# Kernel tuning notes

Measured on AMD Instinct MI355X. Metric: run time of the kernel, lower is better.

The kernel has to match this reference:

```python
import jax, jax.numpy as jnp
import numpy as np

HEADS, DH, M_LAND, PINV_ITERS, LN_EPS = 8, 64, 256, 6, 1e-5


def layer_norm(x, g, b):
    mu = x.mean(-1, keepdims=True)
    var = ((x - mu) ** 2).mean(-1, keepdims=True)
    return (x - mu) * jax.lax.rsqrt(var + LN_EPS) * g + b


def moore_penrose_pinv(x, iters=PINV_ITERS):
    # x: (h, m, m). Iterative Newton-Schulz style pinv (lucidrains).
    abs_x = jnp.abs(x)
    col = abs_x.sum(-1)
    row = abs_x.sum(-2)
    z = jnp.swapaxes(x, -1, -2) / (jnp.max(col) * jnp.max(row))
    I = jnp.eye(x.shape[-1], dtype=x.dtype)
    for _ in range(iters):
        xz = x @ z
        z = 0.25 * z @ (13.0 * I - xz @ (15.0 * I - xz @ (7.0 * I - xz)))
    return z


def nystrom_attention(x, qkv_w, out_w, out_b, res_w):
    # x: (n, dim). No mask, eval mode (dropout off).
    n, dim = x.shape
    pad = (-n) % M_LAND
    xp = jnp.pad(x, ((pad, 0), (0, 0)))  # pad at sequence START, as in original
    n_p = n + pad
    l = n_p // M_LAND  # tokens per landmark
    qkv = xp @ qkv_w  # (n_p, 3*h*dh)
    q, k, v = jnp.split(qkv, 3, axis=-1)
    split = lambda t: t.reshape(n_p, HEADS, DH).transpose(1, 0, 2)  # (h, n_p, dh)
    q, k, v = split(q), split(k), split(v)
    q = q * (DH ** -0.5)
    q_l = q.reshape(HEADS, M_LAND, l, DH).mean(axis=2)  # (h, m, dh)
    k_l = k.reshape(HEADS, M_LAND, l, DH).mean(axis=2)
    sim1 = jnp.einsum('hid,hjd->hij', q, k_l)    # (h, n_p, m)
    sim2 = jnp.einsum('hid,hjd->hij', q_l, k_l)  # (h, m, m)
    sim3 = jnp.einsum('hid,hjd->hij', q_l, k)    # (h, m, n_p)
    a1 = jax.nn.softmax(sim1, axis=-1)
    a2 = jax.nn.softmax(sim2, axis=-1)
    a3 = jax.nn.softmax(sim3, axis=-1)
    a2_inv = moore_penrose_pinv(a2)
    out = a1 @ (a2_inv @ (a3 @ v))  # (h, n_p, dh)
    # residual depthwise conv over sequence dim, kernel 33, per head
    res = jax.lax.conv_general_dilated(
        v[None], res_w, (1, 1), ((16, 16), (0, 0)),
        feature_group_count=HEADS, dimension_numbers=('NCHW', 'OIHW', 'NCHW'))[0]
    out = out + res
    out = out.transpose(1, 0, 2).reshape(n_p, HEADS * DH)
    out = out @ out_w + out_b
    return out[-n:]  # drop the leading pad


def ppeg(x, w7, b7, w5, b5, w3, b3, H, W):
    cls_tok, feat = x[0], x[1:]
    C = feat.shape[1]
    img = feat.T.reshape(1, C, H, W)
    def dw(w, b, p):
        y = jax.lax.conv_general_dilated(
            img, w, (1, 1), ((p, p), (p, p)),
            feature_group_count=C, dimension_numbers=('NCHW', 'OIHW', 'NCHW'))
        return y + b.reshape(1, C, 1, 1)
    out = img + dw(w7, b7, 3) + dw(w5, b5, 2) + dw(w3, b3, 1)
    out = out[0].reshape(C, H * W).T
    return jnp.concatenate([cls_tok[None], out], axis=0)


def forward(h, fc1_w, fc1_b, cls_token, l1_ln_g, l1_ln_b, l1_qkv_w, l1_out_w, l1_out_b, l1_res_w,
            conv7_w, conv7_b, conv5_w, conv5_b, conv3_w, conv3_b,
            l2_ln_g, l2_ln_b, l2_qkv_w, l2_out_w, l2_out_b, l2_res_w,
            norm_g, norm_b, fc2_w, fc2_b):
    x = jax.nn.relu(h @ fc1_w + fc1_b)  # (N, 512)
    N = x.shape[0]
    Hs = Ws = int(np.ceil(np.sqrt(N)))  # N chosen perfect square -> add_length == 0
    x = jnp.concatenate([cls_token, x], axis=0)  # (N+1, 512)
    x = x + nystrom_attention(layer_norm(x, l1_ln_g, l1_ln_b), l1_qkv_w, l1_out_w, l1_out_b, l1_res_w)
    x = ppeg(x, conv7_w, conv7_b, conv5_w, conv5_b, conv3_w, conv3_b, Hs, Ws)
    x = x + nystrom_attention(layer_norm(x, l2_ln_g, l2_ln_b), l2_qkv_w, l2_out_w, l2_out_b, l2_res_w)
    x = layer_norm(x, norm_g, norm_b)[0]  # cls token readout
    return x @ fc2_w + fc2_b  # (n_classes,)


def setup_inputs() -> dict:
    key = jax.random.key(0)
    ks = jax.random.split(key, 16)
    nrm = lambda k, s, sc=0.02: jax.random.normal(k, s, jnp.float32) * sc
    D = 512
    return {
        'h': jax.random.normal(ks[0], (16384, 2048), jnp.float32),
        'fc1_w': nrm(ks[1], (2048, D)), 'fc1_b': jnp.zeros((D,), jnp.float32),
        'cls_token': nrm(ks[2], (1, D), 1.0),
        'l1_ln_g': jnp.ones((D,), jnp.float32), 'l1_ln_b': jnp.zeros((D,), jnp.float32),
        'l1_qkv_w': nrm(ks[3], (D, 3 * D)),
        'l1_out_w': nrm(ks[4], (D, D)), 'l1_out_b': jnp.zeros((D,), jnp.float32),
        'l1_res_w': nrm(ks[5], (HEADS, 1, 33, 1), 0.05),
        'conv7_w': nrm(ks[6], (D, 1, 7, 7), 0.05), 'conv7_b': jnp.zeros((D,), jnp.float32),
        'conv5_w': nrm(ks[7], (D, 1, 5, 5), 0.05), 'conv5_b': jnp.zeros((D,), jnp.float32),
        'conv3_w': nrm(ks[8], (D, 1, 3, 3), 0.05), 'conv3_b': jnp.zeros((D,), jnp.float32),
        'l2_ln_g': jnp.ones((D,), jnp.float32), 'l2_ln_b': jnp.zeros((D,), jnp.float32),
        'l2_qkv_w': nrm(ks[9], (D, 3 * D)),
        'l2_out_w': nrm(ks[10], (D, D)), 'l2_out_b': jnp.zeros((D,), jnp.float32),
        'l2_res_w': nrm(ks[11], (HEADS, 1, 33, 1), 0.05),
        'norm_g': jnp.ones((D,), jnp.float32), 'norm_b': jnp.zeros((D,), jnp.float32),
        'fc2_w': nrm(ks[12], (D, 2)), 'fc2_b': jnp.zeros((2,), jnp.float32),
    }


def reference(h, fc1_w, fc1_b, cls_token, l1_ln_g, l1_ln_b, l1_qkv_w, l1_out_w, l1_out_b, l1_res_w,
              conv7_w, conv7_b, conv5_w, conv5_b, conv3_w, conv3_b,
              l2_ln_g, l2_ln_b, l2_qkv_w, l2_out_w, l2_out_b, l2_res_w,
              norm_g, norm_b, fc2_w, fc2_b):
    return forward(h, fc1_w, fc1_b, cls_token, l1_ln_g, l1_ln_b, l1_qkv_w, l1_out_w, l1_out_b, l1_res_w,
                   conv7_w, conv7_b, conv5_w, conv5_b, conv3_w, conv3_b,
                   l2_ln_g, l2_ln_b, l2_qkv_w, l2_out_w, l2_out_b, l2_res_w,
                   norm_g, norm_b, fc2_w, fc2_b)
```

## Files before the change

### kernel.cpp

```cpp
#include <hip/hip_runtime.h>
#include <cstddef>

#define NROWS 16385
#define NPAD  16640
#define PADT  255
#define DIM   512
#define HEADS 8
#define DH    64
#define NL    256
#define LCH   65
#define LCHUNK 65
#define SLACK 24
#define LDST  40
#define AST   72

typedef short bf16x8 __attribute__((ext_vector_type(8)));
typedef float f32x4  __attribute__((ext_vector_type(4)));

__device__ __forceinline__ float wsum(float v){
#pragma unroll
  for (int o = 32; o; o >>= 1) v += __shfl_xor(v, o);
  return v;
}
__device__ __forceinline__ float wmax(float v){
#pragma unroll
  for (int o = 32; o; o >>= 1) v = fmaxf(v, __shfl_xor(v, o));
  return v;
}

__device__ __forceinline__ int xcd_swz(int orig, int nwg){
  int q = nwg >> 3, r = nwg & 7;
  int x = orig & 7, j = orig >> 3;
  return (x < r ? x*(q+1) : r*(q+1) + (x-r)*q) + j;
}

__device__ __forceinline__ void split2(float x, unsigned short &h, unsigned short &l){
  unsigned ux = __float_as_uint(x);
  unsigned rh = (ux + 0x7FFFu + ((ux >> 16) & 1u)) >> 16;
  h = (unsigned short)rh;
  float fh = __uint_as_float(rh << 16);
  float r = x - fh;
  unsigned ur = __float_as_uint(r);
  unsigned rl = (ur + 0x7FFFu + ((ur >> 16) & 1u)) >> 16;
  l = (unsigned short)rl;
}
__device__ __forceinline__ float bf2f(unsigned short h){
  return __uint_as_float((unsigned)h << 16);
}

__global__ __launch_bounds__(256) void gemm64_sp_kernel(
    const unsigned short* __restrict__ Ah, const unsigned short* __restrict__ Al,
    const unsigned short* __restrict__ Bth, const unsigned short* __restrict__ Btl,
    const unsigned short* __restrict__ IB1h, const unsigned short* __restrict__ IB1l,
    const unsigned short* __restrict__ IB2h, const unsigned short* __restrict__ IB2l,
    float* __restrict__ Cf,
    unsigned short* __restrict__ Crh, unsigned short* __restrict__ Crl,
    unsigned short* __restrict__ Cth, unsigned short* __restrict__ Ctl,
    int M, int N, int K, long sA, long sB, long sC,
    float aAcc, float cDiag, float c1, float c2)
{
  size_t zo = (size_t)blockIdx.z;
  Ah  += zo*sA; Al  += zo*sA;
  Bth += zo*sB; Btl += zo*sB;
  if (IB1h){ IB1h += zo*sA; IB1l += zo*sA; }
  if (IB2h){ IB2h += zo*sA; IB2l += zo*sA; }
  if (Cf)  Cf  += zo*sC;
  if (Crh){ Crh += zo*sC; Crl += zo*sC; }
  if (Cth){ Cth += zo*sC; Ctl += zo*sC; }
  __shared__ unsigned short LAh[64*LDST], LAl[64*LDST], LBh[64*LDST], LBl[64*LDST];
  const int t = threadIdx.x;
  const int wid = t >> 6, lane = t & 63;
  const int wr = wid >> 1, wc = wid & 1;
  const int l15 = lane & 15, kb = lane >> 4;
  const int bm = blockIdx.y << 6, bn = blockIdx.x << 6;
  const int r4 = t >> 2, kc = (t & 3) << 3;
  f32x4 acc[2][2];
#pragma unroll
  for (int i=0;i<2;++i)
#pragma unroll
    for (int j=0;j<2;++j) acc[i][j] = (f32x4){0.f,0.f,0.f,0.f};

  for (int k0 = 0; k0 < K; k0 += 32){
    __syncthreads();
    {
      int lo = r4*LDST + kc;
      *(uint4*)&LAh[lo] = *(const uint4*)&Ah[(size_t)(bm+r4)*K + k0 + kc];
      *(uint4*)&LAl[lo] = *(const uint4*)&Al[(size_t)(bm+r4)*K + k0 + kc];
      *(uint4*)&LBh[lo] = *(const uint4*)&Bth[(size_t)(bn+r4)*K + k0 + kc];
      *(uint4*)&LBl[lo] = *(const uint4*)&Btl[(size_t)(bn+r4)*K + k0 + kc];
    }
    __syncthreads();
    bf16x8 ah[2], al[2], bh[2], bl[2];
#pragma unroll
    for (int r=0;r<2;++r){
      int off = (wr*32 + r*16 + l15)*LDST + kb*8;
      ah[r] = *(const bf16x8*)&LAh[off];
      al[r] = *(const bf16x8*)&LAl[off];
    }
#pragma unroll
    for (int c2v=0;c2v<2;++c2v){
      int off = (wc*32 + c2v*16 + l15)*LDST + kb*8;
      bh[c2v] = *(const bf16x8*)&LBh[off];
      bl[c2v] = *(const bf16x8*)&LBl[off];
    }
#pragma unroll
    for (int r=0;r<2;++r)
#pragma unroll
      for (int c2v=0;c2v<2;++c2v){
        acc[r][c2v] = __builtin_amdgcn_mfma_f32_16x16x32_bf16(ah[r], bh[c2v], acc[r][c2v], 0,0,0);
        acc[r][c2v] = __builtin_amdgcn_mfma_f32_16x16x32_bf16(ah[r], bl[c2v], acc[r][c2v], 0,0,0);
        acc[r][c2v] = __builtin_amdgcn_mfma_f32_16x16x32_bf16(al[r], bh[c2v], acc[r][c2v], 0,0,0);
      }
  }
#pragma unroll
  for (int r=0;r<2;++r){
#pragma unroll
    for (int c2v=0;c2v<2;++c2v){
      int col = bn + wc*32 + c2v*16 + l15;
      int rb  = bm + wr*32 + r*16 + kb*4;
      float v[4];
#pragma unroll
      for (int e=0;e<4;++e){
        float x = aAcc*acc[r][c2v][e];
        int row = rb + e;
        if (cDiag != 0.f && row == col) x += cDiag;
        if (IB1h){
          size_t io = (size_t)row*K + col;
          x += c1*(bf2f(IB1h[io]) + bf2f(IB1l[io]));
        }
        if (IB2h){
          size_t io = (size_t)row*K + col;
          x += c2*(bf2f(IB2h[io]) + bf2f(IB2l[io]));
        }
        v[e] = x;
      }
      if (Cf){
#pragma unroll
        for (int e=0;e<4;++e) Cf[(size_t)(rb+e)*N + col] = v[e];
      }
      if (Crh){
#pragma unroll
        for (int e=0;e<4;++e){
          unsigned short hh, ll;
          split2(v[e], hh, ll);
          Crh[(size_t)(rb+e)*N + col] = hh;
          Crl[(size_t)(rb+e)*N + col] = ll;
        }
      }
      if (Cth){
        unsigned short h4[4], l4[4];
#pragma unroll
        for (int e=0;e<4;++e) split2(v[e], h4[e], l4[e]);
        uint2 uh, ul;
        uh.x = (unsigned)h4[0] | ((unsigned)h4[1]<<16);
        uh.y = (unsigned)h4[2] | ((unsigned)h4[3]<<16);
        ul.x = (unsigned)l4[0] | ((unsigned)l4[1]<<16);
        ul.y = (unsigned)l4[2] | ((unsigned)l4[3]<<16);
        *(uint2*)&Cth[(size_t)col*M + rb] = uh;
        *(uint2*)&Ctl[(size_t)col*M + rb] = ul;
      }
    }
  }
}

__global__ __launch_bounds__(256) void gemm_sb_kernel(
    const unsigned short* __restrict__ Ah, const unsigned short* __restrict__ Al,
    const unsigned short* __restrict__ BTh, const unsigned short* __restrict__ BTl,
    const float* __restrict__ bias, float* __restrict__ C,
    int M, int N, int K, int accum)
{
  __shared__ unsigned short LAh[128*LDST], LAl[128*LDST], LBh[128*LDST], LBl[128*LDST];
  const int t = threadIdx.x;
  const int nwg = gridDim.x * gridDim.y;
  const int orig = blockIdx.y * gridDim.x + blockIdx.x;
  const int wgid = xcd_swz(orig, nwg);
  const int bxi = wgid % gridDim.x, byi = wgid / gridDim.x;
  const int bm = byi << 7, bn = bxi << 7;
  const int wid = t >> 6, lane = t & 63;
  const int wr = wid >> 1, wc = wid & 1;
  const int l15 = lane & 15, kb = lane >> 4;
  const int sr = t >> 1, sc0 = (t & 1) << 4;
  f32x4 acc[4][4];
#pragma unroll
  for (int i=0;i<4;++i)
#pragma unroll
    for (int j=0;j<4;++j) acc[i][j] = (f32x4){0.f,0.f,0.f,0.f};

  const uint4 zz = make_uint4(0,0,0,0);
  for (int k0 = 0; k0 < K; k0 += 32){
    __syncthreads();
    {
      bool av = (bm + sr) < M;
      size_t ga = (size_t)(bm + sr)*K + k0 + sc0;
      uint4 a0 = av ? *(const uint4*)(Ah + ga)     : zz;
      uint4 a1 = av ? *(const uint4*)(Ah + ga + 8) : zz;
      uint4 a2 = av ? *(const uint4*)(Al + ga)     : zz;
      uint4 a3 = av ? *(const uint4*)(Al + ga + 8) : zz;
      size_t gb = (size_t)(bn + sr)*K + k0 + sc0;
      uint4 b0 = *(const uint4*)(BTh + gb);
      uint4 b1 = *(const uint4*)(BTh + gb + 8);
      uint4 b2 = *(const uint4*)(BTl + gb);
      uint4 b3 = *(const uint4*)(BTl + gb + 8);
      int lo = sr*LDST + sc0;
      *(uint4*)&LAh[lo] = a0; *(uint4*)&LAh[lo+8] = a1;
      *(uint4*)&LAl[lo] = a2; *(uint4*)&LAl[lo+8] = a3;
      *(uint4*)&LBh[lo] = b0; *(uint4*)&LBh[lo+8] = b1;
      *(uint4*)&LBl[lo] = b2; *(uint4*)&LBl[lo+8] = b3;
    }
    __syncthreads();
    bf16x8 ah[4], al[4], bh[4], bl[4];
#pragma unroll
    for (int ai=0; ai<4; ++ai){
      int off = (wr*64 + ai*16 + l15)*LDST + kb*8;
      ah[ai] = *(const bf16x8*)&LAh[off];
      al[ai] = *(const bf16x8*)&LAl[off];
    }
#pragma unroll
    for (int bj=0; bj<4; ++bj){
      int off = (wc*64 + bj*16 + l15)*LDST + kb*8;
      bh[bj] = *(const bf16x8*)&LBh[off];
      bl[bj] = *(const bf16x8*)&LBl[off];
    }
#pragma unroll
    for (int ai=0; ai<4; ++ai)
#pragma unroll
      for (int bj=0; bj<4; ++bj){
        acc[ai][bj] = __builtin_amdgcn_mfma_f32_16x16x32_bf16(ah[ai], bh[bj], acc[ai][bj], 0,0,0);
        acc[ai][bj] = __builtin_amdgcn_mfma_f32_16x16x32_bf16(ah[ai], bl[bj], acc[ai][bj], 0,0,0);
        acc[ai][bj] = __builtin_amdgcn_mfma_f32_16x16x32_bf16(al[ai], bh[bj], acc[ai][bj], 0,0,0);
      }
  }
#pragma unroll
  for (int ai=0; ai<4; ++ai){
#pragma unroll
    for (int bj=0; bj<4; ++bj){
      int col = bn + wc*64 + bj*16 + l15;
      float bv = bias ? bias[col] : 0.f;
#pragma unroll
      for (int r=0; r<4; ++r){
        int row = bm + wr*64 + ai*16 + kb*4 + r;
        if (row < M){
          float v = acc[ai][bj][r] + bv;
          if (accum) v += C[(size_t)row*N + col];
          C[(size_t)row*N + col] = v;
        }
      }
    }
  }
}

__global__ __launch_bounds__(256) void gemm_sbf_kernel(
    const float* __restrict__ A,
    const unsigned short* __restrict__ BTh, const unsigned short* __restrict__ BTl,
    const float* __restrict__ bias, float* __restrict__ C,
    int M, int N, int K, int relu)
{
  __shared__ unsigned short LAh[128*LDST], LAl[128*LDST], LBh[128*LDST], LBl[128*LDST];
  const int t = threadIdx.x;
  const int nwg = gridDim.x * gridDim.y;
  const int orig = blockIdx.y * gridDim.x + blockIdx.x;
  const int wgid = xcd_swz(orig, nwg);
  const int bxi = wgid % gridDim.x, byi = wgid / gridDim.x;
  const int bm = byi << 7, bn = bxi << 7;
  const int wid = t >> 6, lane = t & 63;
  const int wr = wid >> 1, wc = wid & 1;
  const int l15 = lane & 15, kb = lane >> 4;
  const int sr = t >> 1, sc0 = (t & 1) << 4;
  f32x4 acc[4][4];
#pragma unroll
  for (int i=0;i<4;++i)
#pragma unroll
    for (int j=0;j<4;++j) acc[i][j] = (f32x4){0.f,0.f,0.f,0.f};

  for (int k0 = 0; k0 < K; k0 += 32){
    __syncthreads();
    {
      const float* ap = A + (size_t)(bm + sr)*K + k0 + sc0;
      float va[16];
      *(float4*)&va[0]  = ((const float4*)ap)[0];
      *(float4*)&va[4]  = ((const float4*)ap)[1];
      *(float4*)&va[8]  = ((const float4*)ap)[2];
      *(float4*)&va[12] = ((const float4*)ap)[3];
      int lo = sr*LDST + sc0;
      unsigned* dh = (unsigned*)&LAh[lo];
      unsigned* dl = (unsigned*)&LAl[lo];
#pragma unroll
      for (int q=0;q<8;++q){
        unsigned short h0,l0,h1,l1;
        split2(va[2*q],   h0, l0);
        split2(va[2*q+1], h1, l1);
        dh[q] = (unsigned)h0 | ((unsigned)h1 << 16);
        dl[q] = (unsigned)l0 | ((unsigned)l1 << 16);
      }
      size_t gb = (size_t)(bn + sr)*K + k0 + sc0;
      uint4 b0 = *(const uint4*)(BTh + gb);
      uint4 b1 = *(const uint4*)(BTh + gb + 8);
      uint4 b2 = *(const uint4*)(BTl + gb);
      uint4 b3 = *(const uint4*)(BTl + gb + 8);
      *(uint4*)&LBh[lo] = b0; *(uint4*)&LBh[lo+8] = b1;
      *(uint4*)&LBl[lo] = b2; *(uint4*)&LBl[lo+8] = b3;
    }
    __syncthreads();
    bf16x8 ah[4], al[4], bh[4], bl[4];
#pragma unroll
    for (int ai=0; ai<4; ++ai){
      int off = (wr*64 + ai*16 + l15)*LDST + kb*8;
      ah[ai] = *(const bf16x8*)&LAh[off];
      al[ai] = *(const bf16x8*)&LAl[off];
    }
#pragma unroll
    for (int bj=0; bj<4; ++bj){
      int off = (wc*64 + bj*16 + l15)*LDST + kb*8;
      bh[bj] = *(const bf16x8*)&LBh[off];
      bl[bj] = *(const bf16x8*)&LBl[off];
// ... 19 lines not shown
        float v = acc[ai][bj][r] + bv;
        if (relu) v = fmaxf(v, 0.f);
        C[(size_t)row*N + col] = v;
      }
    }
  }
}

__global__ void wt_split_T_kernel(const float* __restrict__ W,
                                  unsigned short* __restrict__ BTh,
                                  unsigned short* __restrict__ BTl, int K, int N)
{
  int idx = blockIdx.x*256 + threadIdx.x;
  if (idx >= N*K) return;
  int n = idx / K, k = idx - n*K;
  unsigned short h, l;
  split2(W[(size_t)k*N + n], h, l);
  BTh[idx] = h; BTl[idx] = l;
}

__global__ void att_split_kernel(const float* __restrict__ ATT,
                                 unsigned short* __restrict__ Ah,
                                 unsigned short* __restrict__ Al)
{
  size_t i4 = (size_t)blockIdx.x*256 + threadIdx.x;
  size_t e = i4*4;
  int row = (int)(e >> 9);
  float4 v = make_float4(0.f,0.f,0.f,0.f);
  if (row < NROWS) v = *(const float4*)(ATT + (size_t)PADT*DIM + e);
  unsigned short h0,l0,h1,l1,h2,l2,h3,l3;
  split2(v.x,h0,l0); split2(v.y,h1,l1); split2(v.z,h2,l2); split2(v.w,h3,l3);
  uint2 uh, ul;
  uh.x = (unsigned)h0 | ((unsigned)h1<<16); uh.y = (unsigned)h2 | ((unsigned)h3<<16);
  ul.x = (unsigned)l0 | ((unsigned)l1<<16); ul.y = (unsigned)l2 | ((unsigned)l3<<16);
  *(uint2*)(Ah + e) = uh;
  *(uint2*)(Al + e) = ul;
}

__global__ __launch_bounds__(256) void ln_pad_sb_kernel(
    const float* __restrict__ X, const float* __restrict__ g,
    const float* __restrict__ b, unsigned short* __restrict__ Yh,
    unsigned short* __restrict__ Yl)
{
  int p = blockIdx.x;
  int t = threadIdx.x;
  size_t base = (size_t)p*DIM;
  if (p < PADT){
    Yh[base+t] = 0; Yh[base+t+256] = 0;
    Yl[base+t] = 0; Yl[base+t+256] = 0;
    return;
  }
  const float* xr = X + (size_t)(p-PADT)*DIM;
  float x0 = xr[t], x1 = xr[t+256];
  float s = x0 + x1, sq = x0*x0 + x1*x1;
  s = wsum(s); sq = wsum(sq);
  __shared__ float rs[4], rq[4];
  if ((t&63)==0){ rs[t>>6]=s; rq[t>>6]=sq; }
  __syncthreads();
  float S = rs[0]+rs[1]+rs[2]+rs[3];
  float SQ = rq[0]+rq[1]+rq[2]+rq[3];
  float mu = S * (1.f/DIM);
  float var = SQ * (1.f/DIM) - mu*mu;
  float r = rsqrtf(var + 1e-5f);
  float y0 = (x0-mu)*r*g[t]     + b[t];
  float y1 = (x1-mu)*r*g[t+256] + b[t+256];
  unsigned short h, l;
  split2(y0, h, l); Yh[base+t] = h;     Yl[base+t] = l;
  split2(y1, h, l); Yh[base+t+256] = h; Yl[base+t+256] = l;
}

__global__ void landmarks_kernel(const float* __restrict__ QKV,
                                 float* __restrict__ QL, float* __restrict__ KL,
                                 unsigned short* __restrict__ KLh,
                                 unsigned short* __restrict__ KLl)
{
  int m = blockIdx.x, h = blockIdx.y, d = threadIdx.x;
  float sq = 0.f, sk = 0.f;
  const float* base = QKV + (size_t)(m*LCH)*1536 + (h<<6) + d;
  for (int j = 0; j < LCH; ++j){
    sq += base[0];
    sk += base[512];
    base += 1536;
  }
  size_t off = (((size_t)(h<<8)+m)<<6) + d;
  float klv = sk * (1.f/65.f);
  QL[off] = sq * (0.125f/65.f);
  KL[off] = klv;
  unsigned short hh, ll;
  split2(klv, hh, ll);
  KLh[off] = hh; KLl[off] = ll;
}

__global__ __launch_bounds__(256) void sim2_kernel(
    const float* __restrict__ QL, const float* __restrict__ KL, float* __restrict__ A2)
{
  int m = blockIdx.x, h = blockIdx.y, n = threadIdx.x;
  __shared__ float ql[64];
  __shared__ float red[4];
  if (n < 64) ql[n] = QL[(((h<<8)+m)<<6) + n];
  __syncthreads();
  const float* kl = KL + (size_t)(((h<<8)+n)<<6);
  float s = 0.f;
#pragma unroll
  for (int d=0; d<64; ++d) s += ql[d]*kl[d];
  float mx = wmax(s);
  if ((n&63)==0) red[n>>6] = mx;
  __syncthreads();
  mx = fmaxf(fmaxf(red[0],red[1]), fmaxf(red[2],red[3]));
  float e = __expf(s - mx);
  float sm = wsum(e);
  __syncthreads();
  if ((n&63)==0) red[n>>6] = sm;
  __syncthreads();
  sm = red[0]+red[1]+red[2]+red[3];
  A2[((size_t)((h<<8)+m)<<8) + n] = e/sm;
}

__global__ void crsum_kernel(const float* __restrict__ A2, float* __restrict__ CR)
{
  int b = blockIdx.x, t = threadIdx.x;
  float v;
  if (b < 2048){
    v = fabsf(A2[((size_t)b<<8) + t]);
  } else {
    int r = b - 2048;
    int h = r >> 8, n = r & 255;
    v = fabsf(A2[((size_t)h<<16) + (t<<8) + n]);
  }
  v = wsum(v);
  __shared__ float red[4];
  if ((t&63)==0) red[t>>6]=v;
  __syncthreads();
  if (t==0) CR[b] = red[0]+red[1]+red[2]+red[3];
}
__global__ void maxprod_kernel(const float* __restrict__ CR, float* __restrict__ SCAL)
{
  int t = threadIdx.x;
  float mc = -3e38f, mr = -3e38f;
  for (int i=t; i<2048; i+=256){ mc = fmaxf(mc, CR[i]); mr = fmaxf(mr, CR[2048+i]); }
  mc = wmax(mc); mr = wmax(mr);
  __shared__ float rc[4], rr[4];
  if ((t&63)==0){ rc[t>>6]=mc; rr[t>>6]=mr; }
  __syncthreads();
  if (t==0){
    float a = fmaxf(fmaxf(rc[0],rc[1]),fmaxf(rc[2],rc[3]));
    float b = fmaxf(fmaxf(rr[0],rr[1]),fmaxf(rr[2],rr[3]));
    SCAL[0] = 1.f/(a*b);
  }
}

__global__ void tsplit_kernel(const float* __restrict__ A2, const float* __restrict__ SCAL,
                              unsigned short* __restrict__ A2h, unsigned short* __restrict__ A2l,
                              unsigned short* __restrict__ Zrh, unsigned short* __restrict__ Zrl,
                              unsigned short* __restrict__ Zth, unsigned short* __restrict__ Ztl)
{
  int idx = blockIdx.x*256 + threadIdx.x;
  int h = idx >> 16, rem = idx & 65535, m = rem >> 8, n = rem & 255;
  float a = A2[idx];
  unsigned short hh, ll;
  split2(a, hh, ll);
  A2h[idx] = hh; A2l[idx] = ll;
  float z = a * SCAL[0];
  split2(z, hh, ll);
  Zth[idx] = hh; Ztl[idx] = ll;
  size_t rmo = ((size_t)h<<16) + (n<<8) + m;
  Zrh[rmo] = hh; Zrl[rmo] = ll;
}

__global__ __launch_bounds__(256) void lattn3_kernel(
    const float* __restrict__ QKV, const float* __restrict__ QL,
    float* __restrict__ PACC, float* __restrict__ PML)
{
  const int c = blockIdx.x, lg = blockIdx.y, h = blockIdx.z;
  const int t = threadIdx.x;
  const int w = t >> 6, lane = t & 63;
  const int l15 = lane & 15, kb = lane >> 4;
  __shared__ unsigned short LQh[64*AST], LQl[64*AST];
  __shared__ unsigned short LKh[64*AST], LKl[64*AST];
  __shared__ unsigned short LPh[64*AST], LPl[64*AST];
  const int sr = t >> 2, sc0 = (t & 3) << 4;
  {
    const float* qp = QL + (((size_t)(h*256 + lg*64 + sr)) << 6) + sc0;
    float va[16];
    *(float4*)&va[0]  = ((const float4*)qp)[0];
    *(float4*)&va[4]  = ((const float4*)qp)[1];
    *(float4*)&va[8]  = ((const float4*)qp)[2];
    *(float4*)&va[12] = ((const float4*)qp)[3];
    unsigned* dh = (unsigned*)&LQh[sr*AST + sc0];
    unsigned* dl = (unsigned*)&LQl[sr*AST + sc0];
#pragma unroll
    for (int q=0;q<8;++q){
      unsigned short h0,l0,h1,l1;
      split2(va[2*q],   h0, l0);
      split2(va[2*q+1], h1, l1);
      dh[q] = (unsigned)h0 | ((unsigned)h1 << 16);
      dl[q] = (unsigned)l0 | ((unsigned)l1 << 16);
    }
  }
  float m = -3e38f, l = 0.f;
  f32x4 oacc[4];
#pragma unroll
  for (int i=0;i<4;++i) oacc[i] = (f32x4){0.f,0.f,0.f,0.f};

  for (int s = 0; s < 4; ++s){
    const int kbase = c*256 + s*64;
    __syncthreads();
    {
      const float* kp = QKV + (size_t)(kbase + sr)*1536 + 512 + (h<<6) + sc0;
      float va[16];
      *(float4*)&va[0]  = ((const float4*)kp)[0];
      *(float4*)&va[4]  = ((const float4*)kp)[1];
      *(float4*)&va[8]  = ((const float4*)kp)[2];
      *(float4*)&va[12] = ((const float4*)kp)[3];
      unsigned* dh = (unsigned*)&LKh[sr*AST + sc0];
      unsigned* dl = (unsigned*)&LKl[sr*AST + sc0];
#pragma unroll
      for (int q=0;q<8;++q){
        unsigned short h0,l0,h1,l1;
        split2(va[2*q],   h0, l0);
        split2(va[2*q+1], h1, l1);
        dh[q] = (unsigned)h0 | ((unsigned)h1 << 16);
        dl[q] = (unsigned)l0 | ((unsigned)l1 << 16);
      }
    }
    __syncthreads();
    f32x4 sacc[4];
#pragma unroll
    for (int i=0;i<4;++i) sacc[i] = (f32x4){0.f,0.f,0.f,0.f};
    __builtin_amdgcn_s_setprio(1);
#pragma unroll
    for (int ks = 0; ks < 2; ++ks){
      int qoff = (w*16 + l15)*AST + ks*32 + kb*8;
      bf16x8 bh = *(const bf16x8*)&LQh[qoff];
      bf16x8 bl = *(const bf16x8*)&LQl[qoff];
#pragma unroll
      for (int mi=0; mi<4; ++mi){
        int aoff = (mi*16 + l15)*AST + ks*32 + kb*8;
        bf16x8 ah = *(const bf16x8*)&LKh[aoff];
        bf16x8 al = *(const bf16x8*)&LKl[aoff];
        sacc[mi] = __builtin_amdgcn_mfma_f32_16x16x32_bf16(ah, bh, sacc[mi], 0,0,0);
        sacc[mi] = __builtin_amdgcn_mfma_f32_16x16x32_bf16(ah, bl, sacc[mi], 0,0,0);
        sacc[mi] = __builtin_amdgcn_mfma_f32_16x16x32_bf16(al, bh, sacc[mi], 0,0,0);
      }
    }
    __builtin_amdgcn_s_setprio(0);
    float tm = -3e38f;
#pragma unroll
    for (int mi=0;mi<4;++mi)
#pragma unroll
      for (int e=0;e<4;++e) tm = fmaxf(tm, sacc[mi][e]);
    tm = fmaxf(tm, __shfl_xor(tm, 16));
    tm = fmaxf(tm, __shfl_xor(tm, 32));
    float Mn = fmaxf(m, tm);
    float sc = __expf(m - Mn);
    float ts = 0.f;
    float p[4][4];
#pragma unroll
    for (int mi=0;mi<4;++mi)
#pragma unroll
      for (int e=0;e<4;++e){
        float pv = __expf(sacc[mi][e] - Mn);
        p[mi][e] = pv; ts += pv;
      }
    ts += __shfl_xor(ts, 16);
    ts += __shfl_xor(ts, 32);
    l = l*sc + ts;
    m = Mn;
#pragma unroll
    for (int mi=0;mi<4;++mi)
#pragma unroll
      for (int e=0;e<4;++e) oacc[mi][e] *= sc;
#pragma unroll
    for (int mi=0;mi<4;++mi){
      unsigned short h4[4], l4[4];
#pragma unroll
      for (int e=0;e<4;++e) split2(p[mi][e], h4[e], l4[e]);
      uint2 uh, ul;
      uh.x = (unsigned)h4[0] | ((unsigned)h4[1]<<16);
      uh.y = (unsigned)h4[2] | ((unsigned)h4[3]<<16);
      ul.x = (unsigned)l4[0] | ((unsigned)l4[1]<<16);
      ul.y = (unsigned)l4[2] | ((unsigned)l4[3]<<16);
      int po = (w*16 + l15)*AST + mi*16 + kb*4;
      *(uint2*)&LPh[po] = uh;
      *(uint2*)&LPl[po] = ul;
    }
    __syncthreads();
    {
      const float* vp = QKV + (size_t)(kbase + sr)*1536 + 1024 + (h<<6) + sc0;
      float va[16];
      *(float4*)&va[0]  = ((const float4*)vp)[0];
      *(float4*)&va[4]  = ((const float4*)vp)[1];
      *(float4*)&va[8]  = ((const float4*)vp)[2];
      *(float4*)&va[12] = ((const float4*)vp)[3];
#pragma unroll
      for (int i=0;i<16;++i){
        unsigned short hh, ll;
        split2(va[i], hh, ll);
        LKh[(sc0+i)*AST + sr] = hh;
        LKl[(sc0+i)*AST + sr] = ll;
      }
    }
    __syncthreads();
    __builtin_amdgcn_s_setprio(1);
#pragma unroll
    for (int ks = 0; ks < 2; ++ks){
      int poff = (w*16 + l15)*AST + ks*32 + kb*8;
      bf16x8 pbh = *(const bf16x8*)&LPh[poff];
      bf16x8 pbl = *(const bf16x8*)&LPl[poff];
#pragma unroll
// ... 207 lines not shown
    }
  }
}

__global__ void zero_slack_kernel(float* __restrict__ QKV)
{
  int i = blockIdx.x*256 + threadIdx.x;
  QKV[(size_t)NPAD*1536 + i] = 0.f;
}

__global__ __launch_bounds__(256) void convres2_kernel(
    const float* __restrict__ QKV, const float* __restrict__ rw,
    float* __restrict__ ATT)
{
  const int t = threadIdx.x;
  const int c = blockIdx.y*256 + t;
  const int i0 = PADT + (blockIdx.x << 2);
  const int h = c >> 6;
  float w[33];
#pragma unroll
  for (int k=0;k<33;++k) w[k] = rw[h*33 + k];
  float acc[4] = {0.f,0.f,0.f,0.f};
  const float* vbase = QKV + (size_t)(i0-16)*1536 + 1024 + c;
#pragma unroll
  for (int rr=0; rr<36; ++rr){
    float v = vbase[(size_t)rr*1536];
#pragma unroll
    for (int k=0;k<4;++k){
      int tap = rr - k;
      if (tap >= 0 && tap <= 32) acc[k] += w[tap]*v;
    }
  }
#pragma unroll
  for (int k=0;k<4;++k){
    int i = i0 + k;
    if (i < NPAD) ATT[(size_t)i*DIM + c] += acc[k];
  }
}

__global__ void pad_kernel(const float* __restrict__ X, float* __restrict__ PIM)
{
  int r = blockIdx.x;
  int c = blockIdx.y*256 + threadIdx.x;
  int py = r / 134, px = r - py*134;
  float v = 0.f;
  if (py>=3 && py<131 && px>=3 && px<131)
    v = X[(size_t)(1 + (py-3)*128 + (px-3))*512 + c];
  PIM[(size_t)r*512 + c] = v;
}

__global__ void wtrans_kernel(const float* __restrict__ w7, const float* __restrict__ w5,
                              const float* __restrict__ w3, float* __restrict__ W7T,
                              float* __restrict__ W5T, float* __restrict__ W3T)
{
  int i = blockIdx.x;
  int c = blockIdx.y*256 + threadIdx.x;
  if (i < 49)      W7T[i*512+c]      = w7[c*49+i];
  else if (i < 74) W5T[(i-49)*512+c] = w5[c*25+(i-49)];
  else             W3T[(i-74)*512+c] = w3[c*9+(i-74)];
}

__global__ __launch_bounds__(256) void ppeg2_kernel(
    const float* __restrict__ PIM, const float* __restrict__ W7T,
    const float* __restrict__ W5T, const float* __restrict__ W3T,
    const float* __restrict__ b7, const float* __restrict__ b5,
    const float* __restrict__ b3, float* __restrict__ X2)
{
  const int t = threadIdx.x;
  const int c = blockIdx.z*256 + t;
  const int x = blockIdx.x;
  const int y0 = blockIdx.y << 2;
  float w7r[49], w5r[25], w3r[9];
#pragma unroll
  for (int i=0;i<49;++i) w7r[i] = W7T[i*512 + c];
#pragma unroll
  for (int i=0;i<25;++i) w5r[i] = W5T[i*512 + c];
#pragma unroll
  for (int i=0;i<9;++i)  w3r[i] = W3T[i*512 + c];
  const float bsum = b7[c] + b5[c] + b3[c];
  float acc[4] = {bsum, bsum, bsum, bsum};
  const float* base = PIM + ((size_t)(y0*134 + x))*512 + c;
#pragma unroll
  for (int rr=0; rr<10; ++rr){
#pragma unroll
    for (int cc=0; cc<7; ++cc){
      float v = base[(size_t)(rr*134 + cc)*512];
#pragma unroll
      for (int k=0;k<4;++k){
        const int dy = rr - k - 3, dx = cc - 3;
        if (dy >= -3 && dy <= 3){
          acc[k] += w7r[(dy+3)*7 + (dx+3)] * v;
          if (dy >= -2 && dy <= 2 && dx >= -2 && dx <= 2)
            acc[k] += w5r[(dy+2)*5 + (dx+2)] * v;
          if (dy >= -1 && dy <= 1 && dx >= -1 && dx <= 1)
            acc[k] += w3r[(dy+1)*3 + (dx+1)] * v;
          if (dy == 0 && dx == 0) acc[k] += v;
        }
      }
    }
  }
#pragma unroll
  for (int k=0;k<4;++k)
    X2[(size_t)(1 + (y0+k)*128 + x)*512 + c] = acc[k];
}

__global__ void copy_row_kernel(const float* __restrict__ src, float* __restrict__ dst)
{
  dst[threadIdx.x] = src[threadIdx.x];
}

__global__ void final_kernel(const float* __restrict__ X, const float* __restrict__ g,
                             const float* __restrict__ b, const float* __restrict__ fw,
                             const float* __restrict__ fb, float* __restrict__ out)
{
  int t = threadIdx.x;
  float x0 = X[t], x1 = X[t+256];
  float s = x0 + x1, sq = x0*x0 + x1*x1;
  s = wsum(s); sq = wsum(sq);
  __shared__ float rs[4], rq[4];
  if ((t&63)==0){ rs[t>>6]=s; rq[t>>6]=sq; }
  __syncthreads();
  float S = rs[0]+rs[1]+rs[2]+rs[3];
  float SQ = rq[0]+rq[1]+rq[2]+rq[3];
  float mu = S*(1.f/DIM);
  float var = SQ*(1.f/DIM) - mu*mu;
  float r = rsqrtf(var + 1e-5f);
  float n0 = (x0-mu)*r*g[t]     + b[t];
  float n1 = (x1-mu)*r*g[t+256] + b[t+256];
  float p0 = n0*fw[t*2]   + n1*fw[(t+256)*2];
  float p1 = n0*fw[t*2+1] + n1*fw[(t+256)*2+1];
  p0 = wsum(p0); p1 = wsum(p1);
  __shared__ float r0[4], r1[4];
  if ((t&63)==0){ r0[t>>6]=p0; r1[t>>6]=p1; }
  __syncthreads();
  if (t==0){
    out[0] = r0[0]+r0[1]+r0[2]+r0[3] + fb[0];
    out[1] = r1[0]+r1[1]+r1[2]+r1[3] + fb[1];
  }
}

struct Bufs {
  float *Y, *QKV, *QL, *KL, *A2, *CR, *SCAL, *PACC, *PML, *W7T, *W5T, *W3T;
  unsigned short *Yh, *Yl, *ATh, *ATl, *qBTh, *qBTl, *oBTh, *oBTl, *fBTh, *fBTl;
  unsigned short *A2h, *A2l, *XZrh, *XZrl, *XZth, *XZtl, *Wth, *Wtl, *W2th, *W2tl;
  unsigned short *Z0rh, *Z0rl, *Z0th, *Z0tl, *Z1rh, *Z1rl, *Z1th, *Z1tl;
  unsigned short *TMth, *TMtl, *KLh, *KLl, *BMth, *BMtl;
};

static void attention_layer(float* X, const float* ln_g, const float* ln_b,
                            const float* qkv_w, const float* out_w, const float* out_b,
                            const float* res_w, Bufs& bf, hipStream_t stream)
{
  const long SP = 65536;
  wt_split_T_kernel<<<(1536*512)/256, 256, 0, stream>>>(qkv_w, bf.qBTh, bf.qBTl, 512, 1536);
  wt_split_T_kernel<<<(512*512)/256, 256, 0, stream>>>(out_w, bf.oBTh, bf.oBTl, 512, 512);
  ln_pad_sb_kernel<<<NPAD, 256, 0, stream>>>(X, ln_g, ln_b, bf.Yh, bf.Yl);
  gemm_sb_kernel<<<dim3(12,130),256,0,stream>>>(bf.Yh, bf.Yl, bf.qBTh, bf.qBTl,
      nullptr, bf.QKV, NPAD, 1536, 512, 0);
  landmarks_kernel<<<dim3(NL,HEADS),64,0,stream>>>(bf.QKV, bf.QL, bf.KL, bf.KLh, bf.KLl);
  sim2_kernel<<<dim3(NL,HEADS),256,0,stream>>>(bf.QL, bf.KL, bf.A2);
  crsum_kernel<<<4096,256,0,stream>>>(bf.A2, bf.CR);
  maxprod_kernel<<<1,256,0,stream>>>(bf.CR, bf.SCAL);
  tsplit_kernel<<<2048,256,0,stream>>>(bf.A2, bf.SCAL, bf.A2h, bf.A2l,
      bf.Z0rh, bf.Z0rl, bf.Z0th, bf.Z0tl);
  unsigned short *Zarh=bf.Z0rh, *Zarl=bf.Z0rl, *Zath=bf.Z0th, *Zatl=bf.Z0tl;
  unsigned short *Zbrh=bf.Z1rh, *Zbrl=bf.Z1rl, *Zbth=bf.Z1th, *Zbtl=bf.Z1tl;
  for (int it = 0; it < 6; ++it){
    gemm64_sp_kernel<<<dim3(4,4,8),256,0,stream>>>(bf.A2h, bf.A2l, Zath, Zatl,
        nullptr,nullptr, nullptr,nullptr, nullptr,
        bf.XZrh, bf.XZrl, bf.XZth, bf.XZtl,
        256,256,256, SP,SP,SP, 1.f, 0.f, 0.f, 0.f);
    gemm64_sp_kernel<<<dim3(4,4,8),256,0,stream>>>(bf.XZrh, bf.XZrl, bf.XZth, bf.XZtl,
        bf.XZrh, bf.XZrl, nullptr,nullptr, nullptr,
        nullptr, nullptr, bf.Wth, bf.Wtl,
        256,256,256, SP,SP,SP, -1.f, 0.f, 7.f, 0.f);
    gemm64_sp_kernel<<<dim3(4,4,8),256,0,stream>>>(bf.XZrh, bf.XZrl, bf.Wth, bf.Wtl,
        bf.XZrh, bf.XZrl, nullptr,nullptr, nullptr,
        nullptr, nullptr, bf.W2th, bf.W2tl,
        256,256,256, SP,SP,SP, -1.f, 0.f, 15.f, 0.f);
    gemm64_sp_kernel<<<dim3(4,4,8),256,0,stream>>>(Zarh, Zarl, bf.W2th, bf.W2tl,
        Zarh, Zarl, nullptr,nullptr, nullptr,
        Zbrh, Zbrl, Zbth, Zbtl,
        256,256,256, SP,SP,SP, -0.25f, 0.f, 3.25f, 0.f);
    unsigned short* tp;
    tp=Zarh; Zarh=Zbrh; Zbrh=tp;  tp=Zarl; Zarl=Zbrl; Zbrl=tp;
    tp=Zath; Zath=Zbth; Zbth=tp;  tp=Zatl; Zatl=Zbtl; Zbtl=tp;
  }
  lattn3_kernel<<<dim3(LCHUNK,4,HEADS),256,0,stream>>>(bf.QKV, bf.QL, bf.PACC, bf.PML);
  lattn_combine_kernel<<<2048,64,0,stream>>>(bf.PACC, bf.PML, bf.TMth, bf.TMtl);
  gemm64_sp_kernel<<<dim3(1,4,8),256,0,stream>>>(Zarh, Zarl, bf.TMth, bf.TMtl,
      nullptr,nullptr, nullptr,nullptr, nullptr,
      nullptr, nullptr, bf.BMth, bf.BMtl,
      256,64,256, SP, 16384L, 16384L, 1.f, 0.f, 0.f, 0.f);
  float* ATT = bf.Y;
  attn3_kernel<<<dim3(257,HEADS),256,0,stream>>>(bf.QKV, bf.KLh, bf.KLl,
      bf.BMth, bf.BMtl, ATT);
  convres2_kernel<<<dim3(4097,2),256,0,stream>>>(bf.QKV, res_w, ATT);
  att_split_kernel<<<8256,256,0,stream>>>(ATT, bf.ATh, bf.ATl);
  gemm_sb_kernel<<<dim3(4,129),256,0,stream>>>(bf.ATh, bf.ATl, bf.oBTh, bf.oBTl,
      out_b, X, NROWS, 512, 512, 1);
}

extern "C" void kernel_launch(void* const* d_in, const int* in_sizes, int n_in,
                              void* d_out, int out_size, void* d_ws, size_t ws_size,
                              hipStream_t stream)
{
  (void)in_sizes; (void)n_in; (void)out_size; (void)ws_size;
  const float* h       = (const float*)d_in[0];
  const float* fc1_w   = (const float*)d_in[1];
  const float* fc1_b   = (const float*)d_in[2];
  const float* cls     = (const float*)d_in[3];
  const float* l1_ln_g = (const float*)d_in[4];
  const float* l1_ln_b = (const float*)d_in[5];
  const float* l1_qkv_w= (const float*)d_in[6];
  const float* l1_out_w= (const float*)d_in[7];
  const float* l1_out_b= (const float*)d_in[8];
  const float* l1_res_w= (const float*)d_in[9];
  const float* conv7_w = (const float*)d_in[10];
  const float* conv7_b = (const float*)d_in[11];
  const float* conv5_w = (const float*)d_in[12];
  const float* conv5_b = (const float*)d_in[13];
  const float* conv3_w = (const float*)d_in[14];
  const float* conv3_b = (const float*)d_in[15];
  const float* l2_ln_g = (const float*)d_in[16];
  const float* l2_ln_b = (const float*)d_in[17];
  const float* l2_qkv_w= (const float*)d_in[18];
  const float* l2_out_w= (const float*)d_in[19];
  const float* l2_out_b= (const float*)d_in[20];
  const float* l2_res_w= (const float*)d_in[21];
  const float* norm_g  = (const float*)d_in[22];
  const float* norm_b  = (const float*)d_in[23];
  const float* fc2_w   = (const float*)d_in[24];
  const float* fc2_b   = (const float*)d_in[25];

  float* ws = (float*)d_ws;
  float* X   = ws;                 ws += (size_t)NROWS*DIM;
  float* X2  = ws;                 ws += (size_t)NROWS*DIM;
  Bufs bf;
  bf.Y    = ws;                    ws += (size_t)NPAD*DIM;
  bf.QKV  = ws;                    ws += (size_t)(NPAD+SLACK)*1536;
  bf.QL   = ws;                    ws += HEADS*NL*DH;
  bf.KL   = ws;                    ws += HEADS*NL*DH;
  bf.A2   = ws;                    ws += HEADS*NL*NL;
  bf.CR   = ws;                    ws += 4096;
  bf.SCAL = ws;                    ws += 8;
  bf.PACC = ws;                    ws += (size_t)LCHUNK*HEADS*NL*DH;
  bf.PML  = ws;                    ws += (size_t)LCHUNK*HEADS*NL*2;
  bf.W7T  = ws;                    ws += 49*512;
  bf.W5T  = ws;                    ws += 25*512;
  bf.W3T  = ws;                    ws += 9*512;
  unsigned short* us = (unsigned short*)ws;
  bf.Yh   = us;                    us += (size_t)NPAD*DIM;
  bf.Yl   = us;                    us += (size_t)NPAD*DIM;
  bf.ATh  = us;                    us += (size_t)16512*DIM;
  bf.ATl  = us;                    us += (size_t)16512*DIM;
  bf.qBTh = us;                    us += 1536*512;
  bf.qBTl = us;                    us += 1536*512;
  bf.oBTh = us;                    us += 512*512;
  bf.oBTl = us;                    us += 512*512;
  bf.fBTh = us;                    us += 512*2048;
  bf.fBTl = us;                    us += 512*2048;
  const size_t PL = (size_t)HEADS*NL*NL;
  bf.A2h  = us; us += PL;  bf.A2l  = us; us += PL;
  bf.XZrh = us; us += PL;  bf.XZrl = us; us += PL;
  bf.XZth = us; us += PL;  bf.XZtl = us; us += PL;
  bf.Wth  = us; us += PL;  bf.Wtl  = us; us += PL;
  bf.W2th = us; us += PL;  bf.W2tl = us; us += PL;
  bf.Z0rh = us; us += PL;  bf.Z0rl = us; us += PL;
  bf.Z0th = us; us += PL;  bf.Z0tl = us; us += PL;
  bf.Z1rh = us; us += PL;  bf.Z1rl = us; us += PL;
  bf.Z1th = us; us += PL;  bf.Z1tl = us; us += PL;
  bf.TMth = us; us += (size_t)HEADS*NL*DH;
  bf.TMtl = us; us += (size_t)HEADS*NL*DH;
  bf.KLh  = us; us += (size_t)HEADS*NL*DH;
  bf.KLl  = us; us += (size_t)HEADS*NL*DH;
  bf.BMth = us; us += (size_t)HEADS*NL*DH;
  bf.BMtl = us; us += (size_t)HEADS*NL*DH;
  float* PIM = bf.QKV;

  zero_slack_kernel<<<(SLACK*1536)/256, 256, 0, stream>>>(bf.QKV);
  wtrans_kernel<<<dim3(83,2),256,0,stream>>>(conv7_w, conv5_w, conv3_w,
                                             bf.W7T, bf.W5T, bf.W3T);

  wt_split_T_kernel<<<(512*2048)/256, 256, 0, stream>>>(fc1_w, bf.fBTh, bf.fBTl, 2048, 512);
  gemm_sbf_kernel<<<dim3(4,128),256,0,stream>>>(h, bf.fBTh, bf.fBTl, fc1_b, X + DIM,
      16384, 512, 2048, 1);
  copy_row_kernel<<<1,512,0,stream>>>(cls, X);

  attention_layer(X, l1_ln_g, l1_ln_b, l1_qkv_w, l1_out_w, l1_out_b, l1_res_w, bf, stream);

  pad_kernel<<<dim3(17956,2),256,0,stream>>>(X, PIM);
  ppeg2_kernel<<<dim3(128,32,2),256,0,stream>>>(PIM, bf.W7T, bf.W5T, bf.W3T,
                                                conv7_b, conv5_b, conv3_b, X2);
  copy_row_kernel<<<1,512,0,stream>>>(X, X2);

  attention_layer(X2, l2_ln_g, l2_ln_b, l2_qkv_w, l2_out_w, l2_out_b, l2_res_w, bf, stream);

  final_kernel<<<1,256,0,stream>>>(X2, norm_g, norm_b, fc2_w, fc2_b, (float*)d_out);
}
```

Before: 1.913 ms.

## Fuse pinv Newton-Schulz iterations into one persistent kernel with grid barriers

Replaces the 24 small per-iteration GEMM launches of the Moore-Penrose pinv with a single persistent kernel of 128 blocks that runs all four stages of each of the six iterations. The stages are separated by an atomic-counter grid barrier, and the counter is reset in tsplit. The goal is to remove launch overhead and inter-kernel gaps on tiny 256x256 batched GEMMs. The cost is spin-wait barriers that assume all 128 blocks are co-resident, plus a risk of deadlock or memory-visibility problems. The final Z lands back in the Z0 buffers after an even number of swaps.

Result: slower. 2.958 ms (+54.6%).

```diff
diff --git a/kernel.cpp b/kernel.cpp
--- a/kernel.cpp
+++ b/kernel.cpp
@@ -46,6 +46,17 @@
 }
 __device__ __forceinline__ float bf2f(unsigned short h){
   return __uint_as_float((unsigned)h << 16);
+}
+
+__device__ __forceinline__ void gbar(unsigned* bar, unsigned target){
+  __threadfence();
+  __syncthreads();
+  if (threadIdx.x == 0){
+    atomicAdd(bar, 1u);
+    while (atomicAdd(bar, 0u) < target) __builtin_amdgcn_s_sleep(2);
+  }
+  __syncthreads();
+  __threadfence();
 }
 
 __global__ __launch_bounds__(256) void gemm64_sp_kernel(
@@ -160,6 +171,141 @@
         *(uint2*)&Ctl[(size_t)col*M + rb] = ul;
       }
     }
+  }
+}
+
+__device__ void pinv_stage(
+    const unsigned short* Ah, const unsigned short* Al,
+    const unsigned short* Bth, const unsigned short* Btl,
+    const unsigned short* IBh, const unsigned short* IBl,
+    unsigned short* Crh, unsigned short* Crl,
+    unsigned short* Cth, unsigned short* Ctl,
+    float aAcc, float c1, int bx, int by, int bz)
+{
+  __shared__ unsigned short LAh[64*LDST], LAl[64*LDST], LBh[64*LDST], LBl[64*LDST];
+  const size_t zo = (size_t)bz * 65536;
+  Ah += zo; Al += zo; Bth += zo; Btl += zo;
+  if (IBh){ IBh += zo; IBl += zo; }
+  if (Crh){ Crh += zo; Crl += zo; }
+  if (Cth){ Cth += zo; Ctl += zo; }
+  const int t = threadIdx.x;
+  const int wid = t >> 6, lane = t & 63;
+  const int wr = wid >> 1, wc = wid & 1;
+  const int l15 = lane & 15, kb = lane >> 4;
+  const int bm = by << 6, bn = bx << 6;
+  const int r4 = t >> 2, kc = (t & 3) << 3;
+  f32x4 acc[2][2];
+#pragma unroll
+  for (int i=0;i<2;++i)
+#pragma unroll
+    for (int j=0;j<2;++j) acc[i][j] = (f32x4){0.f,0.f,0.f,0.f};
+
+  for (int k0 = 0; k0 < 256; k0 += 32){
+    __syncthreads();
+    {
+      int lo = r4*LDST + kc;
+      *(uint4*)&LAh[lo] = *(const uint4*)&Ah[(size_t)(bm+r4)*256 + k0 + kc];
+      *(uint4*)&LAl[lo] = *(const uint4*)&Al[(size_t)(bm+r4)*256 + k0 + kc];
+      *(uint4*)&LBh[lo] = *(const uint4*)&Bth[(size_t)(bn+r4)*256 + k0 + kc];
+      *(uint4*)&LBl[lo] = *(const uint4*)&Btl[(size_t)(bn+r4)*256 + k0 + kc];
+    }
+    __syncthreads();
+    bf16x8 ah[2], al[2], bh[2], bl[2];
+#pragma unroll
+    for (int r=0;r<2;++r){
+      int off = (wr*32 + r*16 + l15)*LDST + kb*8;
+      ah[r] = *(const bf16x8*)&LAh[off];
+      al[r] = *(const bf16x8*)&LAl[off];
+    }
+#pragma unroll
+    for (int c2v=0;c2v<2;++c2v){
+      int off = (wc*32 + c2v*16 + l15)*LDST + kb*8;
+      bh[c2v] = *(const bf16x8*)&LBh[off];
+      bl[c2v] = *(const bf16x8*)&LBl[off];
+    }
+#pragma unroll
+    for (int r=0;r<2;++r)
+#pragma unroll
+      for (int c2v=0;c2v<2;++c2v){
+        acc[r][c2v] = __builtin_amdgcn_mfma_f32_16x16x32_bf16(ah[r], bh[c2v], acc[r][c2v], 0,0,0);
+        acc[r][c2v] = __builtin_amdgcn_mfma_f32_16x16x32_bf16(ah[r], bl[c2v], acc[r][c2v], 0,0,0);
+        acc[r][c2v] = __builtin_amdgcn_mfma_f32_16x16x32_bf16(al[r], bh[c2v], acc[r][c2v], 0,0,0);
+      }
+  }
+#pragma unroll
+  for (int r=0;r<2;++r){
+#pragma unroll
+    for (int c2v=0;c2v<2;++c2v){
+      int col = bn + wc*32 + c2v*16 + l15;
+      int rb  = bm + wr*32 + r*16 + kb*4;
+      float v[4];
+#pragma unroll
+      for (int e=0;e<4;++e){
+        float x = aAcc*acc[r][c2v][e];
+        if (IBh){
+          size_t io = (size_t)(rb+e)*256 + col;
+          x += c1*(bf2f(IBh[io]) + bf2f(IBl[io]));
+        }
+        v[e] = x;
+      }
+      if (Crh){
+#pragma unroll
+        for (int e=0;e<4;++e){
+          unsigned short hh, ll;
+          split2(v[e], hh, ll);
+          Crh[(size_t)(rb+e)*256 + col] = hh;
+          Crl[(size_t)(rb+e)*256 + col] = ll;
+        }
+      }
+      if (Cth){
+        unsigned short h4[4], l4[4];
+#pragma unroll
+        for (int e=0;e<4;++e) split2(v[e], h4[e], l4[e]);
+        uint2 uh, ul;
+        uh.x = (unsigned)h4[0] | ((unsigned)h4[1]<<16);
+        uh.y = (unsigned)h4[2] | ((unsigned)h4[3]<<16);
+        ul.x = (unsigned)l4[0] | ((unsigned)l4[1]<<16);
+        ul.y = (unsigned)l4[2] | ((unsigned)l4[3]<<16);
+        *(uint2*)&Cth[(size_t)col*256 + rb] = uh;
+        *(uint2*)&Ctl[(size_t)col*256 + rb] = ul;
+      }
+    }
+  }
+}
+
+__global__ __launch_bounds__(256) void pinv_fused_kernel(
+    const unsigned short* __restrict__ A2h, const unsigned short* __restrict__ A2l,
+    unsigned short* __restrict__ XZrh, unsigned short* __restrict__ XZrl,
+    unsigned short* __restrict__ XZth, unsigned short* __restrict__ XZtl,
+    unsigned short* __restrict__ Wth,  unsigned short* __restrict__ Wtl,
+    unsigned short* __restrict__ W2th, unsigned short* __restrict__ W2tl,
+    unsigned short* __restrict__ Z0rh, unsigned short* __restrict__ Z0rl,
+    unsigned short* __restrict__ Z0th, unsigned short* __restrict__ Z0tl,
+    unsigned short* __restrict__ Z1rh, unsigned short* __restrict__ Z1rl,
+    unsigned short* __restrict__ Z1th, unsigned short* __restrict__ Z1tl,
+    unsigned* __restrict__ bar)
+{
+  const int blk = blockIdx.x;
+  const int bx = blk & 3, by = (blk >> 2) & 3, bz = blk >> 4;
+  unsigned short *Zarh=Z0rh, *Zarl=Z0rl, *Zath=Z0th, *Zatl=Z0tl;
+  unsigned short *Zbrh=Z1rh, *Zbrl=Z1rl, *Zbth=Z1th, *Zbtl=Z1tl;
+  unsigned tgt = 0;
+  for (int it = 0; it < 6; ++it){
+    pinv_stage(A2h,A2l, Zath,Zatl, nullptr,nullptr,
+               XZrh,XZrl, XZth,XZtl, 1.f, 0.f, bx,by,bz);
+    tgt += 128; gbar(bar, tgt);
+    pinv_stage(XZrh,XZrl, XZth,XZtl, XZrh,XZrl,
+               nullptr,nullptr, Wth,Wtl, -1.f, 7.f, bx,by,bz);
+    tgt += 128; gbar(bar, tgt);
+    pinv_stage(XZrh,XZrl, Wth,Wtl, XZrh,XZrl,
+               nullptr,nullptr, W2th,W2tl, -1.f, 15.f, bx,by,bz);
+    tgt += 128; gbar(bar, tgt);
+    pinv_stage(Zarh,Zarl, W2th,W2tl, Zarh,Zarl,
+               Zbrh,Zbrl, Zbth,Zbtl, -0.25f, 3.25f, bx,by,bz);
+    unsigned short* tp;
+    tp=Zarh; Zarh=Zbrh; Zbrh=tp;  tp=Zarl; Zarl=Zbrl; Zbrl=tp;
+    tp=Zath; Zath=Zbth; Zbth=tp;  tp=Zatl; Zatl=Zbtl; Zbtl=tp;
+    if (it < 5){ tgt += 128; gbar(bar, tgt); }
   }
 }
 
@@ -485,9 +631,11 @@
 __global__ void tsplit_kernel(const float* __restrict__ A2, const float* __restrict__ SCAL,
                               unsigned short* __restrict__ A2h, unsigned short* __restrict__ A2l,
                               unsigned short* __restrict__ Zrh, unsigned short* __restrict__ Zrl,
-                              unsigned short* __restrict__ Zth, unsigned short* __restrict__ Ztl)
+                              unsigned short* __restrict__ Zth, unsigned short* __restrict__ Ztl,
+                              unsigned* __restrict__ BAR)
 {
   int idx = blockIdx.x*256 + threadIdx.x;
+  if (idx == 0) BAR[0] = 0u;
   int h = idx >> 16, rem = idx & 65535, m = rem >> 8, n = rem & 255;
   float a = A2[idx];
   unsigned short hh, ll;
@@ -1001,6 +1149,7 @@
                             const float* res_w, Bufs& bf, hipStream_t stream)
 {
   const long SP = 65536;
+  unsigned* BAR = (unsigned*)(bf.SCAL + 4);
   wt_split_T_kernel<<<(1536*512)/256, 256, 0, stream>>>(qkv_w, bf.qBTh, bf.qBTl, 512, 1536);
   wt_split_T_kernel<<<(512*512)/256, 256, 0, stream>>>(out_w, bf.oBTh, bf.oBTl, 512, 512);
   ln_pad_sb_kernel<<<NPAD, 256, 0, stream>>>(X, ln_g, ln_b, bf.Yh, bf.Yl);
@@ -1011,33 +1160,15 @@
   crsum_kernel<<<4096,256,0,stream>>>(bf.A2, bf.CR);
   maxprod_kernel<<<1,256,0,stream>>>(bf.CR, bf.SCAL);
   tsplit_kernel<<<2048,256,0,stream>>>(bf.A2, bf.SCAL, bf.A2h, bf.A2l,
-      bf.Z0rh, bf.Z0rl, bf.Z0th, bf.Z0tl);
-  unsigned short *Zarh=bf.Z0rh, *Zarl=bf.Z0rl, *Zath=bf.Z0th, *Zatl=bf.Z0tl;
-  unsigned short *Zbrh=bf.Z1rh, *Zbrl=bf.Z1rl, *Zbth=bf.Z1th, *Zbtl=bf.Z1tl;
-  for (int it = 0; it < 6; ++it){
-    gemm64_sp_kernel<<<dim3(4,4,8),256,0,stream>>>(bf.A2h, bf.A2l, Zath, Zatl,
-        nullptr,nullptr, nullptr,nullptr, nullptr,
-        bf.XZrh, bf.XZrl, bf.XZth, bf.XZtl,
-        256,256,256, SP,SP,SP, 1.f, 0.f, 0.f, 0.f);
-    gemm64_sp_kernel<<<dim3(4,4,8),256,0,stream>>>(bf.XZrh, bf.XZrl, bf.XZth, bf.XZtl,
-        bf.XZrh, bf.XZrl, nullptr,nullptr, nullptr,
-        nullptr, nullptr, bf.Wth, bf.Wtl,
-        256,256,256, SP,SP,SP, -1.f, 0.f, 7.f, 0.f);
-    gemm64_sp_kernel<<<dim3(4,4,8),256,0,stream>>>(bf.XZrh, bf.XZrl, bf.Wth, bf.Wtl,
-        bf.XZrh, bf.XZrl, nullptr,nullptr, nullptr,
-        nullptr, nullptr, bf.W2th, bf.W2tl,
-        256,256,256, SP,SP,SP, -1.f, 0.f, 15.f, 0.f);
-    gemm64_sp_kernel<<<dim3(4,4,8),256,0,stream>>>(Zarh, Zarl, bf.W2th, bf.W2tl,
-        Zarh, Zarl, nullptr,nullptr, nullptr,
-        Zbrh, Zbrl, Zbth, Zbtl,
-        256,256,256, SP,SP,SP, -0.25f, 0.f, 3.25f, 0.f);
-    unsigned short* tp;
-    tp=Zarh; Zarh=Zbrh; Zbrh=tp;  tp=Zarl; Zarl=Zbrl; Zbrl=tp;
-    tp=Zath; Zath=Zbth; Zbth=tp;  tp=Zatl; Zatl=Zbtl; Zbtl=tp;
-  }
+      bf.Z0rh, bf.Z0rl, bf.Z0th, bf.Z0tl, BAR);
+  pinv_fused_kernel<<<128,256,0,stream>>>(bf.A2h, bf.A2l,
+      bf.XZrh, bf.XZrl, bf.XZth, bf.XZtl,
+      bf.Wth, bf.Wtl, bf.W2th, bf.W2tl,
+      bf.Z0rh, bf.Z0rl, bf.Z0th, bf.Z0tl,
+      bf.Z1rh, bf.Z1rl, bf.Z1th, bf.Z1tl, BAR);
   lattn3_kernel<<<dim3(LCHUNK,4,HEADS),256,0,stream>>>(bf.QKV, bf.QL, bf.PACC, bf.PML);
   lattn_combine_kernel<<<2048,64,0,stream>>>(bf.PACC, bf.PML, bf.TMth, bf.TMtl);
-  gemm64_sp_kernel<<<dim3(1,4,8),256,0,stream>>>(Zarh, Zarl, bf.TMth, bf.TMtl,
+  gemm64_sp_kernel<<<dim3(1,4,8),256,0,stream>>>(bf.Z0rh, bf.Z0rl, bf.TMth, bf.TMtl,
       nullptr,nullptr, nullptr,nullptr, nullptr,
       nullptr, nullptr, bf.BMth, bf.BMtl,
       256,64,256, SP, 16384L, 16384L, 1.f, 0.f, 0.f, 0.f);
```
